# Performance work log

Measured on AMD Instinct MI355X. Metric: run time of the kernel, lower is better.

The kernel has to match this reference:

```python
import jax, jax.numpy as jnp
import numpy as np

B, N, E = 8, 50000, 400000
DIMS = [4, 64, 64, 3]
K = 3
EPS = 1e-5
NEG_SLOPE = 0.01


def _gcn_norm(edge_index, num_nodes):
    # TAGConv uses gcn_norm with unit edge weights and add_self_loops=False.
    row, col = edge_index[0], edge_index[1]
    w = jnp.ones(row.shape[0], dtype=jnp.float32)
    deg = jax.ops.segment_sum(w, col, num_segments=num_nodes)  # in-degree at target
    dis = jnp.where(deg > 0, jnp.power(jnp.maximum(deg, 1.0), -0.5), 0.0)
    return dis[row] * dis[col]  # [E]


def _tag_conv(x, W, b, row, col, norm, num_nodes):
    # x: [B, N, Fin]; W: [K+1, Fin, Fout]; b: [Fout]
    out = jnp.einsum('bnf,fg->bng', x, W[0])
    h = x
    for k in range(1, W.shape[0]):
        msg = h[:, row, :] * norm[None, :, None]            # [B, E, Fin] gather
        h = jnp.zeros((x.shape[0], num_nodes, x.shape[2]), x.dtype).at[:, col, :].add(msg)  # scatter-add
        out = out + jnp.einsum('bnf,fg->bng', h, W[k])
    return out + b


def _batchnorm(x2d, gamma, beta):
    # training-mode BatchNorm1d over batch dim (biased variance, eps=1e-5)
    mean = jnp.mean(x2d, axis=0)
    var = jnp.mean(jnp.square(x2d - mean), axis=0)
    return gamma * (x2d - mean) * jax.lax.rsqrt(var + EPS) + beta


def _leaky_relu(x):
    return jnp.where(x >= 0, x, NEG_SLOPE * x)


def setup_inputs() -> dict:
    key = jax.random.key(0)
    ks = jax.random.split(key, 12)
    inp = {}
    inp['x'] = jax.random.normal(ks[0], (B, N, DIMS[0]), dtype=jnp.float32)
    inp['edge_index'] = jax.random.randint(ks[1], (2, E), 0, N, dtype=jnp.int64)
    inp['val_min'] = jax.random.uniform(ks[2], (N, 3), dtype=jnp.float32) - 1.5
    inp['val_max'] = jax.random.uniform(ks[3], (N, 3), dtype=jnp.float32) + 0.5
    for l in range(3):
        fin, fout = DIMS[l], DIMS[l + 1]
        scale = 1.0 / np.sqrt(fin)
        inp[f'W{l}'] = jax.random.uniform(ks[4 + l], (K + 1, fin, fout), minval=-scale, maxval=scale, dtype=jnp.float32)
        inp[f'b{l}'] = jnp.zeros((fout,), jnp.float32)
    for l in range(2):
        inp[f'gamma{l}'] = jnp.ones((N * DIMS[l + 1],), jnp.float32)
        inp[f'beta{l}'] = jnp.zeros((N * DIMS[l + 1],), jnp.float32)
    return inp


def reference(x, edge_index, val_min, val_max, W0, b0, W1, b1, W2, b2,
              gamma0, beta0, gamma1, beta1):
    row, col = edge_index[0], edge_index[1]
    norm = _gcn_norm(edge_index, N)
    Ws = [W0, W1, W2]
    bs = [b0, b1, b2]
    gammas = [gamma0, gamma1]
    betas = [beta0, beta1]
    out = x
    for layer in range(2):  # num_layers - 1 hidden layers
        out = _tag_conv(out, Ws[layer], bs[layer], row, col, norm, N)
        d = DIMS[layer + 1]
        out = _batchnorm(out.reshape(-1, N * d), gammas[layer], betas[layer]).reshape(-1, N, d)
        out = _leaky_relu(out)
    out = _tag_conv(out, Ws[2], bs[2], row, col, norm, N)  # [B, N, 3]
    # non_linearity: gamma = min + (max - min) / (1 + exp(U))
    return val_min[None] + (val_max - val_min)[None] / (1.0 + jnp.exp(out))
```

## Files before the change

kernel.cpp:

```cpp
#include <hip/hip_runtime.h>
#include <math.h>

constexpr int B = 8;
constexpr int N = 50000;
constexpr int E = 400000;
constexpr float BN_EPS = 1e-5f;
constexpr float NEG = 0.01f;


__device__ __forceinline__ unsigned clamp_src(int s) {
    unsigned u = (unsigned)s;
    return (u < (unsigned)N) ? u : 0u;
}

__device__ __forceinline__ unsigned pack_bf16(float a, float b) {
    unsigned ua = __float_as_uint(a);
    unsigned ub = __float_as_uint(b);
    ua = (ua + 0x7FFFu + ((ua >> 16) & 1u)) >> 16;
    ub = (ub + 0x7FFFu + ((ub >> 16) & 1u)) >> 16;
    return (ub << 16) | (ua & 0xFFFFu);
}
__device__ __forceinline__ float unpack_lo(unsigned u) { return __uint_as_float(u << 16); }
__device__ __forceinline__ float unpack_hi(unsigned u) { return __uint_as_float(u & 0xFFFF0000u); }

__device__ __forceinline__ void store_row64_bf(uint4* p, const float acc[64]) {
#pragma unroll
    for (int q = 0; q < 8; ++q) {
        uint4 v;
        v.x = pack_bf16(acc[q * 8 + 0], acc[q * 8 + 1]);
        v.y = pack_bf16(acc[q * 8 + 2], acc[q * 8 + 3]);
        v.z = pack_bf16(acc[q * 8 + 4], acc[q * 8 + 5]);
        v.w = pack_bf16(acc[q * 8 + 6], acc[q * 8 + 7]);
        p[q] = v;
    }
}


__global__ __launch_bounds__(256) void deg_kernel(const int* __restrict__ col, float* __restrict__ deg) {
    int e = blockIdx.x * blockDim.x + threadIdx.x;
    if (e < E) atomicAdd(&deg[clamp_src(col[e])], 1.0f);
}

__global__ __launch_bounds__(256) void scan1_kernel(const float* __restrict__ deg,
                                                    int* __restrict__ part, int* __restrict__ bsum) {
    __shared__ int sm[4];
    int i = blockIdx.x * blockDim.x + threadIdx.x;
    int v = (i < N) ? (int)deg[i] : 0;
    int lane = threadIdx.x & 63, wv = threadIdx.x >> 6;
    int x = v;
#pragma unroll
    for (int off = 1; off < 64; off <<= 1) {
        int t = __shfl_up(x, off);
        if (lane >= off) x += t;
    }
    if (lane == 63) sm[wv] = x;
    __syncthreads();
    int add = 0;
#pragma unroll
    for (int w = 0; w < 4; ++w) if (w < wv) add += sm[w];
    if (i < N) part[i] = x - v + add;
    if (threadIdx.x == blockDim.x - 1) bsum[blockIdx.x] = x + add;
}

__global__ __launch_bounds__(256) void scan2_kernel(const int* __restrict__ bsum, int* __restrict__ boff,
                                                    int nb, int* __restrict__ rowptr) {
    __shared__ int sm[4];
    int i = threadIdx.x;
    int v = (i < nb) ? bsum[i] : 0;
    int lane = i & 63, wv = i >> 6;
    int x = v;
#pragma unroll
    for (int off = 1; off < 64; off <<= 1) {
        int t = __shfl_up(x, off);
        if (lane >= off) x += t;
    }
    if (lane == 63) sm[wv] = x;
    __syncthreads();
    int add = 0;
#pragma unroll
    for (int w = 0; w < 4; ++w) if (w < wv) add += sm[w];
    if (i < nb) boff[i] = x - v + add;
    if (i == 0) rowptr[N] = E;
}

__global__ __launch_bounds__(256) void scan3_kernel(const int* __restrict__ part, const int* __restrict__ boff,
                                                    int* __restrict__ rowptr) {
    int i = blockIdx.x * blockDim.x + threadIdx.x;
    if (i < N) rowptr[i] = part[i] + boff[blockIdx.x];
}

__global__ __launch_bounds__(256) void fill_kernel(const int* __restrict__ row, const int* __restrict__ col,
                                                   const float* __restrict__ deg, const int* __restrict__ rowptr,
                                                   int* __restrict__ cursor, int* __restrict__ csr_src,
                                                   float* __restrict__ csr_w) {
    int e = blockIdx.x * blockDim.x + threadIdx.x;
    if (e >= E) return;
    unsigned r = clamp_src(row[e]), c = clamp_src(col[e]);
    float dr = deg[r], dc = deg[c];
    float w = (dr > 0.f ? rsqrtf(dr) : 0.f) * (dc > 0.f ? rsqrtf(dc) : 0.f);
    unsigned p = (unsigned)(rowptr[c] + atomicAdd(&cursor[c], 1));
    if (p >= (unsigned)E) p = E - 1;
    csr_src[p] = (int)r;
    csr_w[p] = w;
}


template<bool INBF>
__global__ __launch_bounds__(256) void xprop_kernel(const void* __restrict__ xin, const int* __restrict__ rowptr,
                                                    const int* __restrict__ csr_src, const float* __restrict__ csr_w,
                                                    uint2* __restrict__ xout) {
    int b = blockIdx.x & 7;
    int n = (blockIdx.x >> 3) * blockDim.x + threadIdx.x;
    if (n >= N) return;
    float a0 = 0.f, a1 = 0.f, a2 = 0.f, a3 = 0.f;
    int beg = rowptr[n], end = rowptr[n + 1];
    if (beg < 0) beg = 0;
    if (end > E) end = E;
    for (int i = beg; i < end; ++i) {
        unsigned s = clamp_src(csr_src[i]);
        float w = csr_w[i];
        if constexpr (!INBF) {
            float4 v = *((const float4*)xin + (size_t)b * N + s);
            a0 = fmaf(w, v.x, a0); a1 = fmaf(w, v.y, a1);
            a2 = fmaf(w, v.z, a2); a3 = fmaf(w, v.w, a3);
        } else {
            uint2 v = *((const uint2*)xin + (size_t)b * N + s);
            a0 = fmaf(w, unpack_lo(v.x), a0); a1 = fmaf(w, unpack_hi(v.x), a1);
            a2 = fmaf(w, unpack_lo(v.y), a2); a3 = fmaf(w, unpack_hi(v.y), a3);
        }
    }
    uint2 o;
    o.x = pack_bf16(a0, a1);
    o.y = pack_bf16(a2, a3);
    xout[(size_t)b * N + n] = o;
}


__device__ __forceinline__ void load_xv(const float4* __restrict__ x0, const uint2* __restrict__ x1,
                                        const uint2* __restrict__ x2, const uint2* __restrict__ x3,
                                        size_t ro, float xv[16]) {
    float4 v = x0[ro];
    xv[0] = v.x; xv[1] = v.y; xv[2] = v.z; xv[3] = v.w;
    uint2 u1 = x1[ro], u2 = x2[ro], u3 = x3[ro];
    xv[4] = unpack_lo(u1.x); xv[5] = unpack_hi(u1.x); xv[6] = unpack_lo(u1.y); xv[7] = unpack_hi(u1.y);
    xv[8] = unpack_lo(u2.x); xv[9] = unpack_hi(u2.x); xv[10] = unpack_lo(u2.y); xv[11] = unpack_hi(u2.y);
    xv[12] = unpack_lo(u3.x); xv[13] = unpack_hi(u3.x); xv[14] = unpack_lo(u3.y); xv[15] = unpack_hi(u3.y);
}


__global__ __launch_bounds__(256) void stats_kernel(const float4* __restrict__ x0, const uint2* __restrict__ x1,
                                                    const uint2* __restrict__ x2, const uint2* __restrict__ x3,
                                                    const float* __restrict__ W0,
                                                    const float* __restrict__ gamma, const float* __restrict__ beta,
                                                    unsigned* __restrict__ ss) {
    int gid = blockIdx.x * blockDim.x + threadIdx.x;
    int wave = gid >> 6, lane = gid & 63;
    int n = wave * 8 + (lane >> 3);
    int b = lane & 7;
    if (n >= N) return;
    size_t ro = (size_t)b * N + n;
    float xv[16];
    load_xv(x0, x1, x2, x3, ro, xv);
    float z[64];
#pragma unroll
    for (int f = 0; f < 64; ++f) z[f] = 0.f;
#pragma unroll
    for (int kf = 0; kf < 16; ++kf) {
        float xs = xv[kf];
#pragma unroll
        for (int f = 0; f < 64; ++f)
            z[f] = fmaf(xs, W0[kf * 64 + f], z[f]);
    }
    const float* gp = gamma + (size_t)n * 64;
    const float* bp = beta + (size_t)n * 64;
#pragma unroll
    for (int f = 0; f < 64; ++f) {
        float v = z[f];
        float s = v, s2 = v * v;
        s += __shfl_xor(s, 1);  s += __shfl_xor(s, 2);  s += __shfl_xor(s, 4);
        s2 += __shfl_xor(s2, 1); s2 += __shfl_xor(s2, 2); s2 += __shfl_xor(s2, 4);
        float mean = s * 0.125f;
        float var = fmaf(-mean, mean, s2 * 0.125f);
        float rs = rsqrtf(var + BN_EPS);
        float sc = gp[f] * rs;
        float sh = fmaf(-sc, mean, bp[f]);
        if (b == 0) ss[(size_t)n * 64 + f] = pack_bf16(sc, sh);
    }
}


__device__ __forceinline__ void gather64_bf(const uint4* __restrict__ ub8, int beg, int end,
                                            const int* __restrict__ csr_src, const float* __restrict__ csr_w,
                                            float acc[64]) {
    if (beg < 0) beg = 0;
    if (end > E) end = E;
    for (int i = beg; i < end; ++i) {
        unsigned s = clamp_src(csr_src[i]);
        float w = csr_w[i];
        const uint4* up = ub8 + (size_t)s * 8;
#pragma unroll
        for (int q = 0; q < 8; ++q) {
            uint4 v = up[q];
            acc[q * 8 + 0] = fmaf(w, unpack_lo(v.x), acc[q * 8 + 0]);
            acc[q * 8 + 1] = fmaf(w, unpack_hi(v.x), acc[q * 8 + 1]);
            acc[q * 8 + 2] = fmaf(w, unpack_lo(v.y), acc[q * 8 + 2]);
            acc[q * 8 + 3] = fmaf(w, unpack_hi(v.y), acc[q * 8 + 3]);
            acc[q * 8 + 4] = fmaf(w, unpack_lo(v.z), acc[q * 8 + 4]);
            acc[q * 8 + 5] = fmaf(w, unpack_hi(v.z), acc[q * 8 + 5]);
            acc[q * 8 + 6] = fmaf(w, unpack_lo(v.w), acc[q * 8 + 6]);
            acc[q * 8 + 7] = fmaf(w, unpack_hi(v.w), acc[q * 8 + 7]);
        }
    }
}


template<int MODE>
__global__ __launch_bounds__(256) void hopR_kernel(const uint4* __restrict__ u_in, const int* __restrict__ rowptr,
                                                   const int* __restrict__ csr_src, const float* __restrict__ csr_w,
                                                   const float4* __restrict__ x0, const uint2* __restrict__ x1,
                                                   const uint2* __restrict__ x2, const uint2* __restrict__ x3,
                                                   const float* __restrict__ W0, const unsigned* __restrict__ ss,
                                                   const float* __restrict__ Wk, const float* __restrict__ bias,
                                                   uint4* __restrict__ u_out) {
    int b = blockIdx.x & 7;
    int n = (blockIdx.x >> 3) * blockDim.x + threadIdx.x;
    if (n >= N) return;
    size_t ro = (size_t)b * N + n;
    float xv[16];
    load_xv(x0, x1, x2, x3, ro, xv);
    float acc[64];
    if constexpr (MODE == 2) {
#pragma unroll
        for (int f = 0; f < 64; ++f) acc[f] = bias[f];
    } else {
#pragma unroll
        for (int f = 0; f < 64; ++f) acc[f] = 0.f;
    }
    if constexpr (MODE > 0)
        gather64_bf(u_in + (size_t)b * N * 8, rowptr[n], rowptr[n + 1], csr_src, csr_w, acc);
    const unsigned* ssp = ss + (size_t)n * 64;
#pragma unroll 1
    for (int kq = 0; kq < 16; ++kq) {
        uint4 sq = *(const uint4*)(ssp + kq * 4);
        unsigned sqa[4] = {sq.x, sq.y, sq.z, sq.w};
#pragma unroll
        for (int j = 0; j < 4; ++j) {
            int k = kq * 4 + j;
            float z = 0.f;
#pragma unroll
            for (int kf = 0; kf < 16; ++kf)
                z = fmaf(xv[kf], W0[kf * 64 + k], z);
            float h = fmaf(z, unpack_lo(sqa[j]), unpack_hi(sqa[j]));
            h = (h >= 0.f) ? h : NEG * h;
            const float* wr = Wk + k * 64;
#pragma unroll
            for (int c = 0; c < 64; ++c)
                acc[c] = fmaf(h, wr[c], acc[c]);
        }
    }
    store_row64_bf(u_out + ro * 8, acc);
}


__global__ __launch_bounds__(256) void bn_project_kernel(const uint4* __restrict__ z,
                                                         const float* __restrict__ gamma, const float* __restrict__ beta,
                                                         const float* __restrict__ W2, float* __restrict__ y) {
    int gid = blockIdx.x * blockDim.x + threadIdx.x;
    int wave = gid >> 6, lane = gid & 63;
    int n = wave * 8 + (lane >> 3);
    int b = lane & 7;
    if (n >= N) return;
    float acc[64];
    const uint4* zp = z + ((size_t)b * N + n) * 8;
#pragma unroll
    for (int q = 0; q < 8; ++q) {
        uint4 v = zp[q];
        acc[q * 8 + 0] = unpack_lo(v.x); acc[q * 8 + 1] = unpack_hi(v.x);
        acc[q * 8 + 2] = unpack_lo(v.y); acc[q * 8 + 3] = unpack_hi(v.y);
        acc[q * 8 + 4] = unpack_lo(v.z); acc[q * 8 + 5] = unpack_hi(v.z);
        acc[q * 8 + 6] = unpack_lo(v.w); acc[q * 8 + 7] = unpack_hi(v.w);
    }
    const float* gp = gamma + (size_t)n * 64;
    const float* bp = beta + (size_t)n * 64;
#pragma unroll
    for (int f = 0; f < 64; ++f) {
        float v = acc[f];
        float s = v, s2 = v * v;
        s += __shfl_xor(s, 1);  s += __shfl_xor(s, 2);  s += __shfl_xor(s, 4);
        s2 += __shfl_xor(s2, 1); s2 += __shfl_xor(s2, 2); s2 += __shfl_xor(s2, 4);
        float mean = s * 0.125f;
        float var = fmaf(-mean, mean, s2 * 0.125f);
        float xn = (v - mean) * rsqrtf(var + BN_EPS);
        float o = fmaf(gp[f], xn, bp[f]);
        acc[f] = (o >= 0.f) ? o : NEG * o;
    }
    size_t bn3 = ((size_t)b * N + n) * 3;
#pragma unroll
    for (int k = 0; k < 4; ++k) {
#pragma unroll
        for (int c = 0; c < 3; ++c) {
            float s = 0.f;
#pragma unroll
            for (int f = 0; f < 64; ++f)
                s = fmaf(acc[f], W2[k * 192 + f * 3 + c], s);
            y[(size_t)k * B * N * 3 + bn3 + c] = s;
        }
    }
}


__global__ __launch_bounds__(256) void qprop_kernel(const float* __restrict__ vin, const int* __restrict__ rowptr,
                                                    const int* __restrict__ csr_src, const float* __restrict__ csr_w,
                                                    const float* __restrict__ add, float* __restrict__ vout) {
    int b = blockIdx.x & 7;
    int n = (blockIdx.x >> 3) * blockDim.x + threadIdx.x;
    if (n >= N) return;
    float a0 = 0.f, a1 = 0.f, a2 = 0.f;
    int beg = rowptr[n], end = rowptr[n + 1];
    if (beg < 0) beg = 0;
    if (end > E) end = E;
    const float* base = vin + (size_t)b * N * 3;
    for (int i = beg; i < end; ++i) {
        unsigned s = clamp_src(csr_src[i]);
        float w = csr_w[i];
        const float* p = base + (size_t)s * 3;
        a0 = fmaf(w, p[0], a0);
        a1 = fmaf(w, p[1], a1);
        a2 = fmaf(w, p[2], a2);
    }
    const float* ap = add + ((size_t)b * N + n) * 3;
    float* op = vout + ((size_t)b * N + n) * 3;
    op[0] = a0 + ap[0];
    op[1] = a1 + ap[1];
    op[2] = a2 + ap[2];
}

__global__ __launch_bounds__(256) void qfinal_kernel(const float* __restrict__ vin, const int* __restrict__ rowptr,
                                                     const int* __restrict__ csr_src, const float* __restrict__ csr_w,
                                                     const float* __restrict__ y0, const float* __restrict__ b2,
                                                     const float* __restrict__ vmin, const float* __restrict__ vmax,
                                                     float* __restrict__ out) {
    int b = blockIdx.x & 7;
    int n = (blockIdx.x >> 3) * blockDim.x + threadIdx.x;
    if (n >= N) return;
    float a0 = 0.f, a1 = 0.f, a2 = 0.f;
    int beg = rowptr[n], end = rowptr[n + 1];
    if (beg < 0) beg = 0;
    if (end > E) end = E;
    const float* base = vin + (size_t)b * N * 3;
    for (int i = beg; i < end; ++i) {
        unsigned s = clamp_src(csr_src[i]);
        float w = csr_w[i];
        const float* p = base + (size_t)s * 3;
        a0 = fmaf(w, p[0], a0);
        a1 = fmaf(w, p[1], a1);
        a2 = fmaf(w, p[2], a2);
    }
    size_t bn3 = ((size_t)b * N + n) * 3;
    const float* yp = y0 + bn3;
    float g0 = a0 + yp[0] + b2[0];
    float g1 = a1 + yp[1] + b2[1];
    float g2 = a2 + yp[2] + b2[2];
    float mn0 = vmin[n * 3 + 0], mx0 = vmax[n * 3 + 0];
    float mn1 = vmin[n * 3 + 1], mx1 = vmax[n * 3 + 1];
    float mn2 = vmin[n * 3 + 2], mx2 = vmax[n * 3 + 2];
    float* op = out + bn3;
    op[0] = mn0 + (mx0 - mn0) / (1.f + expf(g0));
    op[1] = mn1 + (mx1 - mn1) / (1.f + expf(g1));
    op[2] = mn2 + (mx2 - mn2) / (1.f + expf(g2));
}


extern "C" void kernel_launch(void* const* d_in, const int* in_sizes, int n_in,
                              void* d_out, int out_size, void* d_ws, size_t ws_size,
                              hipStream_t stream) {
    const float* x      = (const float*)d_in[0];
    const int*   ei     = (const int*)d_in[1];
    const int*   rowi   = ei;
    const int*   coli   = ei + E;
    const float* vmin   = (const float*)d_in[2];
    const float* vmax   = (const float*)d_in[3];
    const float* W0     = (const float*)d_in[4];
    const float* W1     = (const float*)d_in[6];
    const float* b1v    = (const float*)d_in[7];
    const float* W2     = (const float*)d_in[8];
    const float* b2v    = (const float*)d_in[9];
    const float* gamma0 = (const float*)d_in[10];
    const float* beta0  = (const float*)d_in[11];
    const float* gamma1 = (const float*)d_in[12];
    const float* beta1  = (const float*)d_in[13];
    float* out = (float*)d_out;

    const size_t BN3  = (size_t)B * N * 3;
    const size_t UFL  = (size_t)B * N * 32;
    const size_t XBFL = (size_t)B * N * 2;

    auto rnd = [](size_t nf) { return (nf + 63) & ~(size_t)63; };
    size_t off = 0;
    auto alloc = [&](size_t nfloats) -> float* {
        float* p = (float*)d_ws + off;
        off += rnd(nfloats);
        return p;
    };
    float* deg     = alloc(N);
    float* csr_w   = alloc(E);
    int*   rowptr  = (int*)alloc(N + 1);
    int*   part    = (int*)alloc(N);
    int*   bsum    = (int*)alloc(256);
    int*   boff    = (int*)alloc(256);
    int*   cursor  = (int*)alloc(N);
    int*   csr_src = (int*)alloc(E);
    uint2* xb1     = (uint2*)alloc(XBFL);
    uint2* xb2     = (uint2*)alloc(XBFL);
    uint2* xb3     = (uint2*)alloc(XBFL);
    unsigned* ss   = (unsigned*)alloc((size_t)N * 64);
    float* u_a     = alloc(UFL);
    float* u_b     = alloc(UFL);
    float* y   = u_a;
    float* v_a = u_a + rnd(4 * BN3);
    float* v_b = v_a + rnd(BN3);

    const int GE  = (E + 255) / 256;
    const int GN  = (N + 255) / 256;
    const int GT  = (B * N + 255) / 256;
    const int GB8 = GN * 8;
    dim3 blk(256);

    hipMemsetAsync(deg, 0, N * sizeof(float), stream);
    hipMemsetAsync(cursor, 0, N * sizeof(int), stream);
    deg_kernel<<<GE, blk, 0, stream>>>(coli, deg);
    scan1_kernel<<<GN, blk, 0, stream>>>(deg, part, bsum);
    scan2_kernel<<<1, blk, 0, stream>>>(bsum, boff, GN, rowptr);
    scan3_kernel<<<GN, blk, 0, stream>>>(part, boff, rowptr);
    fill_kernel<<<GE, blk, 0, stream>>>(rowi, coli, deg, rowptr, cursor, csr_src, csr_w);

    xprop_kernel<false><<<GB8, blk, 0, stream>>>(x,   rowptr, csr_src, csr_w, xb1);
    xprop_kernel<true><<<GB8, blk, 0, stream>>>(xb1, rowptr, csr_src, csr_w, xb2);
    xprop_kernel<true><<<GB8, blk, 0, stream>>>(xb2, rowptr, csr_src, csr_w, xb3);
    stats_kernel<<<GT, blk, 0, stream>>>((const float4*)x, xb1, xb2, xb3, W0, gamma0, beta0, ss);

    hopR_kernel<0><<<GB8, blk, 0, stream>>>(nullptr, rowptr, csr_src, csr_w,
                                            (const float4*)x, xb1, xb2, xb3, W0, ss,
                                            W1 + 3 * 4096, nullptr, (uint4*)u_a);
    hopR_kernel<1><<<GB8, blk, 0, stream>>>((const uint4*)u_a, rowptr, csr_src, csr_w,
                                            (const float4*)x, xb1, xb2, xb3, W0, ss,
                                            W1 + 2 * 4096, nullptr, (uint4*)u_b);
    hopR_kernel<1><<<GB8, blk, 0, stream>>>((const uint4*)u_b, rowptr, csr_src, csr_w,
                                            (const float4*)x, xb1, xb2, xb3, W0, ss,
                                            W1 + 1 * 4096, nullptr, (uint4*)u_a);
    hopR_kernel<2><<<GB8, blk, 0, stream>>>((const uint4*)u_a, rowptr, csr_src, csr_w,
                                            (const float4*)x, xb1, xb2, xb3, W0, ss,
                                            W1, b1v, (uint4*)u_b);
    bn_project_kernel<<<GT, blk, 0, stream>>>((const uint4*)u_b, gamma1, beta1, W2, y);

    qprop_kernel<<<GB8, blk, 0, stream>>>(y + 3 * BN3, rowptr, csr_src, csr_w, y + 2 * BN3, v_a);
    qprop_kernel<<<GB8, blk, 0, stream>>>(v_a, rowptr, csr_src, csr_w, y + 1 * BN3, v_b);
    qfinal_kernel<<<GB8, blk, 0, stream>>>(v_b, rowptr, csr_src, csr_w, y, b2v, vmin, vmax, out);
}
```

Baseline: 1.090 ms.

## Materialize layer-1 activations once and split hop kernels into half-batch passes

Instead of recomputing the layer-0 output (x-projection, batchnorm scale/shift, leaky ReLU) inside every hop kernel, a new kernel writes the activated layer-1 input h1 once in bf16. The hop kernels then do only the gather plus a dense 64x64 update that reads h1. Batches run in two halves of four to shrink the working buffers and let them alias the xprop scratch. The stats and bn_project kernels are remapped so eight lanes share a node and reduce the projection with shuffles. This removes repeated 16x64 recomputation per hop, at the cost of an extra bf16 h1 buffer, more kernel launches, and twice as many hop passes with half-size grids.

```diff
diff --git a/kernel.cpp b/kernel.cpp
--- a/kernel.cpp
+++ b/kernel.cpp
@@ -148,44 +148,54 @@
 }
 
 
-__global__ __launch_bounds__(256) void stats_kernel(const float4* __restrict__ x0, const uint2* __restrict__ x1,
-                                                    const uint2* __restrict__ x2, const uint2* __restrict__ x3,
-                                                    const float* __restrict__ W0,
-                                                    const float* __restrict__ gamma, const float* __restrict__ beta,
-                                                    unsigned* __restrict__ ss) {
+__global__ __launch_bounds__(256) void build_h1_kernel(const float4* __restrict__ x0, const uint2* __restrict__ x1,
+                                                       const uint2* __restrict__ x2, const uint2* __restrict__ x3,
+                                                       const float* __restrict__ W0,
+                                                       const float* __restrict__ gamma, const float* __restrict__ beta,
+                                                       uint4* __restrict__ h1) {
     int gid = blockIdx.x * blockDim.x + threadIdx.x;
-    int wave = gid >> 6, lane = gid & 63;
-    int n = wave * 8 + (lane >> 3);
-    int b = lane & 7;
-    if (n >= N) return;
-    size_t ro = (size_t)b * N + n;
+    int node = gid >> 6;
+    int lane = gid & 63;
+    int fg = lane >> 3, b = lane & 7;
+    if (node >= N) return;
+    size_t ro = (size_t)b * N + node;
     float xv[16];
     load_xv(x0, x1, x2, x3, ro, xv);
-    float z[64];
-#pragma unroll
-    for (int f = 0; f < 64; ++f) z[f] = 0.f;
+    float z[8];
+#pragma unroll
+    for (int j = 0; j < 8; ++j) z[j] = 0.f;
 #pragma unroll
     for (int kf = 0; kf < 16; ++kf) {
+        const float* wr = W0 + kf * 64 + fg * 8;
+        float4 wa = *(const float4*)wr;
+        float4 wb = *(const float4*)(wr + 4);
         float xs = xv[kf];
-#pragma unroll
-        for (int f = 0; f < 64; ++f)
-            z[f] = fmaf(xs, W0[kf * 64 + f], z[f]);
-    }
-    const float* gp = gamma + (size_t)n * 64;
-    const float* bp = beta + (size_t)n * 64;
-#pragma unroll
-    for (int f = 0; f < 64; ++f) {
-        float v = z[f];
+        z[0] = fmaf(xs, wa.x, z[0]); z[1] = fmaf(xs, wa.y, z[1]);
+        z[2] = fmaf(xs, wa.z, z[2]); z[3] = fmaf(xs, wa.w, z[3]);
+        z[4] = fmaf(xs, wb.x, z[4]); z[5] = fmaf(xs, wb.y, z[5]);
+        z[6] = fmaf(xs, wb.z, z[6]); z[7] = fmaf(xs, wb.w, z[7]);
+    }
+    const float* gp = gamma + (size_t)node * 64 + fg * 8;
+    const float* bp = beta + (size_t)node * 64 + fg * 8;
+    float h[8];
+#pragma unroll
+    for (int j = 0; j < 8; ++j) {
+        float v = z[j];
         float s = v, s2 = v * v;
         s += __shfl_xor(s, 1);  s += __shfl_xor(s, 2);  s += __shfl_xor(s, 4);
         s2 += __shfl_xor(s2, 1); s2 += __shfl_xor(s2, 2); s2 += __shfl_xor(s2, 4);
         float mean = s * 0.125f;
         float var = fmaf(-mean, mean, s2 * 0.125f);
         float rs = rsqrtf(var + BN_EPS);
-        float sc = gp[f] * rs;
-        float sh = fmaf(-sc, mean, bp[f]);
-        if (b == 0) ss[(size_t)n * 64 + f] = pack_bf16(sc, sh);
-    }
+        float o = fmaf(gp[j] * rs, v - mean, bp[j]);
+        h[j] = (o >= 0.f) ? o : NEG * o;
+    }
+    uint4 o;
+    o.x = pack_bf16(h[0], h[1]);
+    o.y = pack_bf16(h[2], h[3]);
+    o.z = pack_bf16(h[4], h[5]);
+    o.w = pack_bf16(h[6], h[7]);
+    h1[ro * 8 + fg] = o;
 }
 
 
@@ -213,21 +223,40 @@
     }
 }
 
+__device__ __forceinline__ void dense64_bf(const uint4* __restrict__ hp8, const float* __restrict__ W, float acc[64]) {
+#pragma unroll 1
+    for (int kk = 0; kk < 4; ++kk) {
+        float hreg[16];
+        uint4 va = hp8[kk * 2], vb = hp8[kk * 2 + 1];
+        hreg[0] = unpack_lo(va.x); hreg[1] = unpack_hi(va.x);
+        hreg[2] = unpack_lo(va.y); hreg[3] = unpack_hi(va.y);
+        hreg[4] = unpack_lo(va.z); hreg[5] = unpack_hi(va.z);
+        hreg[6] = unpack_lo(va.w); hreg[7] = unpack_hi(va.w);
+        hreg[8] = unpack_lo(vb.x); hreg[9] = unpack_hi(vb.x);
+        hreg[10] = unpack_lo(vb.y); hreg[11] = unpack_hi(vb.y);
+        hreg[12] = unpack_lo(vb.z); hreg[13] = unpack_hi(vb.z);
+        hreg[14] = unpack_lo(vb.w); hreg[15] = unpack_hi(vb.w);
+        const float* Wp = W + kk * 16 * 64;
+#pragma unroll
+        for (int k = 0; k < 16; ++k) {
+            float hv = hreg[k];
+#pragma unroll
+            for (int c = 0; c < 64; ++c)
+                acc[c] = fmaf(hv, Wp[k * 64 + c], acc[c]);
+        }
+    }
+}
+
 
 template<int MODE>
-__global__ __launch_bounds__(256) void hopR_kernel(const uint4* __restrict__ u_in, const int* __restrict__ rowptr,
+__global__ __launch_bounds__(256) void hopM_kernel(const uint4* __restrict__ u_in, const int* __restrict__ rowptr,
                                                    const int* __restrict__ csr_src, const float* __restrict__ csr_w,
-                                                   const float4* __restrict__ x0, const uint2* __restrict__ x1,
-                                                   const uint2* __restrict__ x2, const uint2* __restrict__ x3,
-                                                   const float* __restrict__ W0, const unsigned* __restrict__ ss,
+                                                   const uint4* __restrict__ h1, int b0,
                                                    const float* __restrict__ Wk, const float* __restrict__ bias,
                                                    uint4* __restrict__ u_out) {
-    int b = blockIdx.x & 7;
-    int n = (blockIdx.x >> 3) * blockDim.x + threadIdx.x;
+    int bl = blockIdx.x & 3;
+    int n = (blockIdx.x >> 2) * blockDim.x + threadIdx.x;
     if (n >= N) return;
-    size_t ro = (size_t)b * N + n;
-    float xv[16];
-    load_xv(x0, x1, x2, x3, ro, xv);
     float acc[64];
     if constexpr (MODE == 2) {
 #pragma unroll
@@ -237,74 +266,64 @@
         for (int f = 0; f < 64; ++f) acc[f] = 0.f;
     }
     if constexpr (MODE > 0)
-        gather64_bf(u_in + (size_t)b * N * 8, rowptr[n], rowptr[n + 1], csr_src, csr_w, acc);
-    const unsigned* ssp = ss + (size_t)n * 64;
-#pragma unroll 1
-    for (int kq = 0; kq < 16; ++kq) {
-        uint4 sq = *(const uint4*)(ssp + kq * 4);
-        unsigned sqa[4] = {sq.x, sq.y, sq.z, sq.w};
-#pragma unroll
-        for (int j = 0; j < 4; ++j) {
-            int k = kq * 4 + j;
-            float z = 0.f;
-#pragma unroll
-            for (int kf = 0; kf < 16; ++kf)
-                z = fmaf(xv[kf], W0[kf * 64 + k], z);
-            float h = fmaf(z, unpack_lo(sqa[j]), unpack_hi(sqa[j]));
-            h = (h >= 0.f) ? h : NEG * h;
-            const float* wr = Wk + k * 64;
-#pragma unroll
-            for (int c = 0; c < 64; ++c)
-                acc[c] = fmaf(h, wr[c], acc[c]);
-        }
-    }
-    store_row64_bf(u_out + ro * 8, acc);
-}
-
-
-__global__ __launch_bounds__(256) void bn_project_kernel(const uint4* __restrict__ z,
+        gather64_bf(u_in + (size_t)bl * N * 8, rowptr[n], rowptr[n + 1], csr_src, csr_w, acc);
+    dense64_bf(h1 + ((size_t)(b0 + bl) * N + n) * 8, Wk, acc);
+    store_row64_bf(u_out + ((size_t)bl * N + n) * 8, acc);
+}
+
+
+__global__ __launch_bounds__(256) void bn_project_kernel(const uint4* __restrict__ zlo, const uint4* __restrict__ zhi,
                                                          const float* __restrict__ gamma, const float* __restrict__ beta,
                                                          const float* __restrict__ W2, float* __restrict__ y) {
     int gid = blockIdx.x * blockDim.x + threadIdx.x;
-    int wave = gid >> 6, lane = gid & 63;
-    int n = wave * 8 + (lane >> 3);
-    int b = lane & 7;
-    if (n >= N) return;
-    float acc[64];
-    const uint4* zp = z + ((size_t)b * N + n) * 8;
-#pragma unroll
-    for (int q = 0; q < 8; ++q) {
-        uint4 v = zp[q];
-        acc[q * 8 + 0] = unpack_lo(v.x); acc[q * 8 + 1] = unpack_hi(v.x);
-        acc[q * 8 + 2] = unpack_lo(v.y); acc[q * 8 + 3] = unpack_hi(v.y);
-        acc[q * 8 + 4] = unpack_lo(v.z); acc[q * 8 + 5] = unpack_hi(v.z);
-        acc[q * 8 + 6] = unpack_lo(v.w); acc[q * 8 + 7] = unpack_hi(v.w);
-    }
-    const float* gp = gamma + (size_t)n * 64;
-    const float* bp = beta + (size_t)n * 64;
-#pragma unroll
-    for (int f = 0; f < 64; ++f) {
-        float v = acc[f];
-        float s = v, s2 = v * v;
+    int node = gid >> 6;
+    int lane = gid & 63;
+    int fg = lane >> 3, b = lane & 7;
+    if (node >= N) return;
+    const uint4* zp = (b < 4) ? (zlo + ((size_t)b * N + node) * 8)
+                              : (zhi + ((size_t)(b - 4) * N + node) * 8);
+    uint4 v = zp[fg];
+    float h[8] = {unpack_lo(v.x), unpack_hi(v.x), unpack_lo(v.y), unpack_hi(v.y),
+                  unpack_lo(v.z), unpack_hi(v.z), unpack_lo(v.w), unpack_hi(v.w)};
+    const float* gp = gamma + (size_t)node * 64 + fg * 8;
+    const float* bp = beta + (size_t)node * 64 + fg * 8;
+#pragma unroll
+    for (int j = 0; j < 8; ++j) {
+        float val = h[j];
+        float s = val, s2 = val * val;
         s += __shfl_xor(s, 1);  s += __shfl_xor(s, 2);  s += __shfl_xor(s, 4);
         s2 += __shfl_xor(s2, 1); s2 += __shfl_xor(s2, 2); s2 += __shfl_xor(s2, 4);
         float mean = s * 0.125f;
         float var = fmaf(-mean, mean, s2 * 0.125f);
-        float xn = (v - mean) * rsqrtf(var + BN_EPS);
-        float o = fmaf(gp[f], xn, bp[f]);
-        acc[f] = (o >= 0.f) ? o : NEG * o;
-    }
-    size_t bn3 = ((size_t)b * N + n) * 3;
+        float rs = rsqrtf(var + BN_EPS);
+        float o = fmaf(gp[j] * rs, val - mean, bp[j]);
+        h[j] = (o >= 0.f) ? o : NEG * o;
+    }
+    float p[12];
 #pragma unroll
     for (int k = 0; k < 4; ++k) {
 #pragma unroll
         for (int c = 0; c < 3; ++c) {
             float s = 0.f;
 #pragma unroll
-            for (int f = 0; f < 64; ++f)
-                s = fmaf(acc[f], W2[k * 192 + f * 3 + c], s);
-            y[(size_t)k * B * N * 3 + bn3 + c] = s;
+            for (int j = 0; j < 8; ++j)
+                s = fmaf(h[j], W2[k * 192 + (fg * 8 + j) * 3 + c], s);
+            p[k * 3 + c] = s;
         }
+    }
+#pragma unroll
+    for (int t = 8; t < 64; t <<= 1) {
+#pragma unroll
+        for (int i = 0; i < 12; ++i)
+            p[i] += __shfl_xor(p[i], t);
+    }
+    if (fg == 0) {
+        size_t bn3 = ((size_t)b * N + node) * 3;
+#pragma unroll
+        for (int k = 0; k < 4; ++k)
+#pragma unroll
+            for (int c = 0; c < 3; ++c)
+                y[(size_t)k * B * N * 3 + bn3 + c] = p[k * 3 + c];
     }
 }
 
@@ -392,7 +411,8 @@
     float* out = (float*)d_out;
 
     const size_t BN3  = (size_t)B * N * 3;
-    const size_t UFL  = (size_t)B * N * 32;
+    const size_t H1FL = (size_t)B * N * 32;
+    const size_t UCFL = (size_t)4 * N * 32;
     const size_t XBFL = (size_t)B * N * 2;
 
     auto rnd = [](size_t nf) { return (nf + 63) & ~(size_t)63; };
@@ -410,20 +430,22 @@
     int*   boff    = (int*)alloc(256);
     int*   cursor  = (int*)alloc(N);
     int*   csr_src = (int*)alloc(E);
-    uint2* xb1     = (uint2*)alloc(XBFL);
-    uint2* xb2     = (uint2*)alloc(XBFL);
-    uint2* xb3     = (uint2*)alloc(XBFL);
-    unsigned* ss   = (unsigned*)alloc((size_t)N * 64);
-    float* u_a     = alloc(UFL);
-    float* u_b     = alloc(UFL);
-    float* y   = u_a;
-    float* v_a = u_a + rnd(4 * BN3);
+    float* h1      = alloc(H1FL);
+    float* uA      = alloc(UCFL);
+    float* uB      = alloc(UCFL);
+    float* uC      = alloc(UCFL);
+    uint2* xb1 = (uint2*)uC;
+    uint2* xb2 = (uint2*)(uC + XBFL);
+    uint2* xb3 = (uint2*)(uC + 2 * XBFL);
+    float* y   = h1;
+    float* v_a = h1 + rnd(4 * BN3);
     float* v_b = v_a + rnd(BN3);
 
     const int GE  = (E + 255) / 256;
     const int GN  = (N + 255) / 256;
-    const int GT  = (B * N + 255) / 256;
     const int GB8 = GN * 8;
+    const int GH4 = GN * 4;
+    const int GW  = (N * 64) / 256;
     dim3 blk(256);
 
     hipMemsetAsync(deg, 0, N * sizeof(float), stream);
@@ -437,21 +459,28 @@
     xprop_kernel<false><<<GB8, blk, 0, stream>>>(x,   rowptr, csr_src, csr_w, xb1);
     xprop_kernel<true><<<GB8, blk, 0, stream>>>(xb1, rowptr, csr_src, csr_w, xb2);
     xprop_kernel<true><<<GB8, blk, 0, stream>>>(xb2, rowptr, csr_src, csr_w, xb3);
-    stats_kernel<<<GT, blk, 0, stream>>>((const float4*)x, xb1, xb2, xb3, W0, gamma0, beta0, ss);
-
-    hopR_kernel<0><<<GB8, blk, 0, stream>>>(nullptr, rowptr, csr_src, csr_w,
-                                            (const float4*)x, xb1, xb2, xb3, W0, ss,
-                                            W1 + 3 * 4096, nullptr, (uint4*)u_a);
-    hopR_kernel<1><<<GB8, blk, 0, stream>>>((const uint4*)u_a, rowptr, csr_src, csr_w,
-                                            (const float4*)x, xb1, xb2, xb3, W0, ss,
-                                            W1 + 2 * 4096, nullptr, (uint4*)u_b);
-    hopR_kernel<1><<<GB8, blk, 0, stream>>>((const uint4*)u_b, rowptr, csr_src, csr_w,
-                                            (const float4*)x, xb1, xb2, xb3, W0, ss,
-                                            W1 + 1 * 4096, nullptr, (uint4*)u_a);
-    hopR_kernel<2><<<GB8, blk, 0, stream>>>((const uint4*)u_a, rowptr, csr_src, csr_w,
-                                            (const float4*)x, xb1, xb2, xb3, W0, ss,
-                                            W1, b1v, (uint4*)u_b);
-    bn_project_kernel<<<GT, blk, 0, stream>>>((const uint4*)u_b, gamma1, beta1, W2, y);
+    build_h1_kernel<<<GW, blk, 0, stream>>>((const float4*)x, xb1, xb2, xb3, W0, gamma0, beta0, (uint4*)h1);
+
+    hopM_kernel<0><<<GH4, blk, 0, stream>>>(nullptr, rowptr, csr_src, csr_w,
+                                            (const uint4*)h1, 0, W1 + 3 * 4096, nullptr, (uint4*)uA);
+    hopM_kernel<1><<<GH4, blk, 0, stream>>>((const uint4*)uA, rowptr, csr_src, csr_w,
+                                            (const uint4*)h1, 0, W1 + 2 * 4096, nullptr, (uint4*)uB);
+    hopM_kernel<1><<<GH4, blk, 0, stream>>>((const uint4*)uB, rowptr, csr_src, csr_w,
+                                            (const uint4*)h1, 0, W1 + 1 * 4096, nullptr, (uint4*)uA);
+    hopM_kernel<2><<<GH4, blk, 0, stream>>>((const uint4*)uA, rowptr, csr_src, csr_w,
+                                            (const uint4*)h1, 0, W1, b1v, (uint4*)uC);
+
+    hopM_kernel<0><<<GH4, blk, 0, stream>>>(nullptr, rowptr, csr_src, csr_w,
+                                            (const uint4*)h1, 4, W1 + 3 * 4096, nullptr, (uint4*)uA);
+    hopM_kernel<1><<<GH4, blk, 0, stream>>>((const uint4*)uA, rowptr, csr_src, csr_w,
+                                            (const uint4*)h1, 4, W1 + 2 * 4096, nullptr, (uint4*)uB);
+    hopM_kernel<1><<<GH4, blk, 0, stream>>>((const uint4*)uB, rowptr, csr_src, csr_w,
+                                            (const uint4*)h1, 4, W1 + 1 * 4096, nullptr, (uint4*)uA);
+    hopM_kernel<2><<<GH4, blk, 0, stream>>>((const uint4*)uA, rowptr, csr_src, csr_w,
+                                            (const uint4*)h1, 4, W1, b1v, (uint4*)uB);
+
+    bn_project_kernel<<<GW, blk, 0, stream>>>((const uint4*)uC, (const uint4*)uB,
+                                              gamma1, beta1, W2, y);
 
     qprop_kernel<<<GB8, blk, 0, stream>>>(y + 3 * BN3, rowptr, csr_src, csr_w, y + 2 * BN3, v_a);
     qprop_kernel<<<GB8, blk, 0, stream>>>(v_a, rowptr, csr_src, csr_w, y + 1 * BN3, v_b);
```

After: 1.006 ms. 7.7% less time.
